# Kernel optimization log

Hardware: AMD Instinct MI355X
Metric: run time of the kernel (lower is better)

Reference implementation:

```python
import jax, jax.numpy as jnp
import numpy as np

B, L, D = 4, 512, 768          # batch, seq, d_model
NL, DI, N, K, R = 12, 1536, 16, 4, 48  # layers, d_inner, d_state, d_conv, dt_rank
V, P = 50257, 1024             # vocab, positions
EPS = 1e-5


def setup_inputs() -> dict:
    key = jax.random.key(0)
    ks = jax.random.split(key, 12)
    p = lambda i, shape, s=0.02: jax.random.normal(ks[i], shape, jnp.float32) * s
    return {
        "input_ids": jax.random.randint(ks[0], (B, L), 0, V),
        "wte": p(1, (V, D)),
        "wpe": p(2, (P, D)),
        "ln_g": jnp.ones((NL, D), jnp.float32),
        "ln_b": jnp.zeros((NL, D), jnp.float32),
        "in_W": p(3, (NL, 2 * DI, D)),
        "conv_W": p(4, (NL, DI, K), 0.2),
        "conv_b": jnp.zeros((NL, DI), jnp.float32),
        "xp_W": p(5, (NL, R + 2 * N, DI)),
        "dt_W": p(6, (NL, DI, R), 0.1),
        "dt_b": p(7, (NL, DI), 0.5),
        # Mamba S4D-real init: A = -exp(A_log), A_log = log(1..N)
        "A_log": jnp.tile(jnp.log(jnp.arange(1, N + 1, dtype=jnp.float32)), (NL, DI, 1)),
        "Dres": jnp.ones((NL, DI), jnp.float32),
        "out_W": p(8, (NL, D, DI)),
        "nf_g": jnp.ones((D,), jnp.float32),
        "nf_b": jnp.zeros((D,), jnp.float32),
        "fin_g": jnp.ones((D,), jnp.float32),
        "fin_b": jnp.zeros((D,), jnp.float32),
    }


def layer_norm(x, g, b):
    mu = jnp.mean(x, -1, keepdims=True)
    var = jnp.mean((x - mu) ** 2, -1, keepdims=True)
    return (x - mu) * jax.lax.rsqrt(var + EPS) * g + b


def causal_conv(x, w, b):
    # x: (B, L, DI); depthwise causal conv, kernel K, left pad K-1, truncate to L
    xt = jnp.transpose(x, (0, 2, 1))  # (B, DI, L)
    y = jax.lax.conv_general_dilated(
        xt, w[:, None, :], (1,), [(K - 1, 0)],
        feature_group_count=DI, dimension_numbers=("NCH", "OIH", "NCH"))
    return jnp.transpose(y + b[None, :, None], (0, 2, 1))


def selective_scan(u, delta, A, Bm, Cm):
    # u, delta: (B, L, DI); A: (DI, N); Bm, Cm: (B, L, N)
    def step(h, inp):
        u_t, d_t, b_t, c_t = inp  # (B,DI), (B,DI), (B,N), (B,N)
        dA = jnp.exp(d_t[:, :, None] * A)            # (B, DI, N)
        h = h * dA + (d_t * u_t)[:, :, None] * b_t[:, None, :]
        y = jnp.einsum("bdn,bn->bd", h, c_t)
        return h, y

    h0 = jnp.zeros((u.shape[0], DI, N), u.dtype)
    xs = (jnp.swapaxes(u, 0, 1), jnp.swapaxes(delta, 0, 1),
          jnp.swapaxes(Bm, 0, 1), jnp.swapaxes(Cm, 0, 1))
    _, ys = jax.lax.scan(step, h0, xs)               # ys: (L, B, DI)
    return jnp.swapaxes(ys, 0, 1)


def mamba_mixer(x, inW, cW, cb, xpW, dtW, dtb, a_log, dres, outW):
    xz = jnp.einsum("bld,ed->ble", x, inW)           # (B, L, 2*DI)
    xi, z = jnp.split(xz, 2, axis=-1)
    xi = jax.nn.silu(causal_conv(xi, cW, cb))
    dbl = jnp.einsum("bld,ed->ble", xi, xpW)         # (B, L, R+2N)
    dt, Bm, Cm = dbl[..., :R], dbl[..., R:R + N], dbl[..., R + N:]
    delta = jax.nn.softplus(jnp.einsum("blr,dr->bld", dt, dtW) + dtb)
    A = -jnp.exp(a_log)
    y = selective_scan(xi, delta, A, Bm, Cm) + xi * dres
    y = y * jax.nn.silu(z)
    return jnp.einsum("ble,de->bld", y, outW)


def reference(input_ids, wte, wpe, ln_g, ln_b, in_W, conv_W, conv_b, xp_W,
              dt_W, dt_b, A_log, Dres, out_W, nf_g, nf_b, fin_g, fin_b):
    emb = wte[input_ids] + wpe[: input_ids.shape[1]]  # (B, L, D); dropout=identity (eval)
    hidden, residual = emb, None
    for i in range(NL):
        residual = hidden if residual is None else hidden + residual
        h = layer_norm(residual, ln_g[i], ln_b[i])
        hidden = mamba_mixer(h, in_W[i], conv_W[i], conv_b[i], xp_W[i],
                             dt_W[i], dt_b[i], A_log[i], Dres[i], out_W[i])
    residual = hidden + residual
    out = layer_norm(residual, nf_g, nf_b)   # MixerModel.norm_f
    return layer_norm(out, fin_g, fin_b)     # decoder self.norm
```

## Files before the change

### kernel.cpp

```cpp
#include <hip/hip_runtime.h>

#define BB 4
#define LL 512
#define DD 768
#define NLAYER 12
#define DI 1536
#define NS 16
#define KC 4
#define RR 48
#define MROWS (BB*LL)
#define E2 (2*DI)
#define EPSV 1e-5f
#define CH2 16
#define LC2 (LL/CH2)

typedef __attribute__((ext_vector_type(8))) short bf16x8;
typedef __attribute__((ext_vector_type(4))) float f32x4;

#define GLL16(g, l) __builtin_amdgcn_global_load_lds( \
    (const __attribute__((address_space(1))) void*)(g), \
    (__attribute__((address_space(3))) void*)(l), 16, 0, 0)

__device__ inline ushort f2bf(float f) {
  union { float f; unsigned u; } v; v.f = f;
  unsigned u = v.u;
  unsigned r = (u + 0x7fffu + ((u >> 16) & 1u)) >> 16;
  return (ushort)r;
}
__device__ inline float bf2f(ushort u) {
  union { unsigned u; float f; } v; v.u = ((unsigned)u) << 16; return v.f;
}

__global__ __launch_bounds__(256) void k_embed(const int* __restrict__ ids,
    const float* __restrict__ wte, const float* __restrict__ wpe,
    float* __restrict__ resid) {
  const int nd4 = DD / 4;
  int i = blockIdx.x * 256 + threadIdx.x;
  if (i >= MROWS * nd4) return;
  int m = i / nd4, d4 = i - m * nd4;
  int l = m & (LL - 1);
  int tok = ids[m];
  float4 a = ((const float4*)wte)[(size_t)tok * nd4 + d4];
  float4 b = ((const float4*)wpe)[(size_t)l * nd4 + d4];
  float4 o; o.x = a.x + b.x; o.y = a.y + b.y; o.z = a.z + b.z; o.w = a.w + b.w;
  ((float4*)resid)[i] = o;
}

__device__ inline float block_sum(float v, volatile float* red) {
  #pragma unroll
  for (int o = 32; o > 0; o >>= 1) v += __shfl_down(v, o);
  if ((threadIdx.x & 63) == 0) red[threadIdx.x >> 6] = v;
  __syncthreads();
  float t = red[0] + red[1] + red[2] + red[3];
  __syncthreads();
  return t;
}

__global__ __launch_bounds__(256) void k_ln(const float* __restrict__ h0,
    const float* __restrict__ h1,
    float* __restrict__ resid, const float* __restrict__ g, const float* __restrict__ b,
    ushort* __restrict__ hbf, int addHidden) {
  __shared__ float red[4];
  int m = blockIdx.x, t = threadIdx.x;
  size_t base = (size_t)m * DD;
  float x0 = resid[base + t], x1 = resid[base + t + 256], x2 = resid[base + t + 512];
  if (addHidden) {
    x0 += h0[base + t]       + h1[base + t];
    x1 += h0[base + t + 256] + h1[base + t + 256];
    x2 += h0[base + t + 512] + h1[base + t + 512];
    resid[base + t] = x0; resid[base + t + 256] = x1; resid[base + t + 512] = x2;
  }
  float S  = block_sum(x0 + x1 + x2, red);
  float S2 = block_sum(x0*x0 + x1*x1 + x2*x2, red);
  float mu = S * (1.f / DD);
  float var = S2 * (1.f / DD) - mu * mu;
  float rs = rsqrtf(var + EPSV);
  hbf[base + t]       = f2bf((x0 - mu) * rs * g[t]       + b[t]);
  hbf[base + t + 256] = f2bf((x1 - mu) * rs * g[t + 256] + b[t + 256]);
  hbf[base + t + 512] = f2bf((x2 - mu) * rs * g[t + 512] + b[t + 512]);
}

template<int OM>
__global__ __launch_bounds__(256) void k_gemm128(const ushort* __restrict__ A,
    const ushort* __restrict__ Bw, void* __restrict__ Cv, int N, int K, int kSteps) {
  __shared__ ushort lA[128 * 32];
  __shared__ ushort lB[128 * 32];
  int tid = threadIdx.x;
  int wid = tid >> 6, lane = tid & 63;
  int tm = blockIdx.y * 128, tn = blockIdx.x * 128;
  int kBase = blockIdx.z * kSteps * 32;
  int wr = (wid >> 1) * 64, wc = (wid & 1) * 64;
  int fr = lane & 15, kg = lane >> 4;
  int srow = lane >> 2;
  int scol = (lane & 3) * 8;
  f32x4 acc[4][4];
  #pragma unroll
  for (int mi = 0; mi < 4; ++mi)
    #pragma unroll
    for (int ni = 0; ni < 4; ++ni)
      acc[mi][ni] = {0.f, 0.f, 0.f, 0.f};

  int rs0 = wid * 2, rs1 = wid * 2 + 1;
  for (int ks = 0; ks < kSteps; ++ks) {
    int k0 = kBase + ks * 32;
    GLL16(A  + (size_t)(tm + rs0 * 16 + srow) * K + k0 + scol, &lA[rs0 * 512]);
    GLL16(A  + (size_t)(tm + rs1 * 16 + srow) * K + k0 + scol, &lA[rs1 * 512]);
    GLL16(Bw + (size_t)(tn + rs0 * 16 + srow) * K + k0 + scol, &lB[rs0 * 512]);
    GLL16(Bw + (size_t)(tn + rs1 * 16 + srow) * K + k0 + scol, &lB[rs1 * 512]);
    __syncthreads();
    bf16x8 af[4], bf[4];
    #pragma unroll
    for (int mi = 0; mi < 4; ++mi)
      af[mi] = *(const bf16x8*)&lA[(wr + mi * 16 + fr) * 32 + kg * 8];
    #pragma unroll
    for (int ni = 0; ni < 4; ++ni)
      bf[ni] = *(const bf16x8*)&lB[(wc + ni * 16 + fr) * 32 + kg * 8];
    #pragma unroll
    for (int mi = 0; mi < 4; ++mi)
      #pragma unroll
      for (int ni = 0; ni < 4; ++ni)
        acc[mi][ni] = __builtin_amdgcn_mfma_f32_16x16x32_bf16(af[mi], bf[ni], acc[mi][ni], 0, 0, 0);
    __syncthreads();
  }
  int crow0 = tm + wr + kg * 4;
  int ccol0 = tn + wc + fr;
  if (OM == 0) {
    float* C = (float*)Cv + (size_t)blockIdx.z * ((size_t)gridDim.y * 128) * N;
    #pragma unroll
    for (int mi = 0; mi < 4; ++mi)
      #pragma unroll
      for (int ni = 0; ni < 4; ++ni)
        #pragma unroll
        for (int j = 0; j < 4; ++j)
          C[(size_t)(crow0 + mi * 16 + j) * N + ccol0 + ni * 16] = acc[mi][ni][j];
  } else {
    ushort* C = (ushort*)Cv;
    #pragma unroll
    for (int mi = 0; mi < 4; ++mi)
      #pragma unroll
      for (int ni = 0; ni < 4; ++ni)
        #pragma unroll
        for (int j = 0; j < 4; ++j)
          C[(size_t)(crow0 + mi * 16 + j) * N + ccol0 + ni * 16] = f2bf(acc[mi][ni][j]);
  }
}

__global__ __launch_bounds__(256) void k_gemm64_part(const ushort* __restrict__ A,
    const ushort* __restrict__ Bw, float* __restrict__ Cp, int N, int K, int kSteps) {
  __shared__ short lA[64][40];
  __shared__ short lB[64][40];
  int tid = threadIdx.x;
  int tm = blockIdx.y * 64, tn = blockIdx.x * 64;
  int kBase = blockIdx.z * kSteps * 32;
  int M = gridDim.y * 64;
  float* C = Cp + (size_t)blockIdx.z * M * N;
  int wid = tid >> 6, lane = tid & 63;
  int wr = (wid >> 1) * 32, wc = (wid & 1) * 32;
  int fr = lane & 15, kg = lane >> 4;
  int ldr = tid >> 2, ldc = (tid & 3) * 8;
  f32x4 acc[2][2];
  #pragma unroll
  for (int mi = 0; mi < 2; ++mi)
    #pragma unroll
    for (int ni = 0; ni < 2; ++ni)
      acc[mi][ni] = {0.f, 0.f, 0.f, 0.f};

  for (int ks = 0; ks < kSteps; ++ks) {
    int k0 = kBase + ks * 32;
    __syncthreads();
    bf16x8 va = *(const bf16x8*)(A + (size_t)(tm + ldr) * K + k0 + ldc);
    short z = 0;
    bf16x8 vb = {z, z, z, z, z, z, z, z};
    int brow = tn + ldr;
    if (brow < N) vb = *(const bf16x8*)(Bw + (size_t)brow * K + k0 + ldc);
    *(bf16x8*)&lA[ldr][ldc] = va;
    *(bf16x8*)&lB[ldr][ldc] = vb;
    __syncthreads();
    bf16x8 a0 = *(const bf16x8*)&lA[wr + fr][kg * 8];
    bf16x8 a1 = *(const bf16x8*)&lA[wr + 16 + fr][kg * 8];
    bf16x8 b0 = *(const bf16x8*)&lB[wc + fr][kg * 8];
    bf16x8 b1 = *(const bf16x8*)&lB[wc + 16 + fr][kg * 8];
    acc[0][0] = __builtin_amdgcn_mfma_f32_16x16x32_bf16(a0, b0, acc[0][0], 0, 0, 0);
    acc[0][1] = __builtin_amdgcn_mfma_f32_16x16x32_bf16(a0, b1, acc[0][1], 0, 0, 0);
    acc[1][0] = __builtin_amdgcn_mfma_f32_16x16x32_bf16(a1, b0, acc[1][0], 0, 0, 0);
    acc[1][1] = __builtin_amdgcn_mfma_f32_16x16x32_bf16(a1, b1, acc[1][1], 0, 0, 0);
  }
  int crow0 = tm + wr + kg * 4;
  int ccol0 = tn + wc + fr;
  #pragma unroll
  for (int mi = 0; mi < 2; ++mi)
    #pragma unroll
    for (int ni = 0; ni < 2; ++ni) {
      int cc = ccol0 + ni * 16;
      if (cc < N) {
        #pragma unroll
        for (int j = 0; j < 4; ++j)
          C[(size_t)(crow0 + mi * 16 + j) * N + cc] = acc[mi][ni][j];
      }
    }
}

__global__ __launch_bounds__(256) void k_gemm64_dt(const ushort* __restrict__ A,
    const ushort* __restrict__ Bw, float* __restrict__ delta,
    const float* __restrict__ dtb, int N, int K) {
  __shared__ short lA[64][40];
  __shared__ short lB[64][40];
  int tid = threadIdx.x;
  int tm = blockIdx.y * 64, tn = blockIdx.x * 64;
  int wid = tid >> 6, lane = tid & 63;
  int wr = (wid >> 1) * 32, wc = (wid & 1) * 32;
  int fr = lane & 15, kg = lane >> 4;
  int ldr = tid >> 2, ldc = (tid & 3) * 8;
  f32x4 acc[2][2];
  #pragma unroll
  for (int mi = 0; mi < 2; ++mi)
    #pragma unroll
    for (int ni = 0; ni < 2; ++ni)
      acc[mi][ni] = {0.f, 0.f, 0.f, 0.f};

  for (int k0 = 0; k0 < K; k0 += 32) {
    __syncthreads();
    bf16x8 va = *(const bf16x8*)(A + (size_t)(tm + ldr) * K + k0 + ldc);
    bf16x8 vb = *(const bf16x8*)(Bw + (size_t)(tn + ldr) * K + k0 + ldc);
    *(bf16x8*)&lA[ldr][ldc] = va;
    *(bf16x8*)&lB[ldr][ldc] = vb;
    __syncthreads();
    bf16x8 a0 = *(const bf16x8*)&lA[wr + fr][kg * 8];
    bf16x8 a1 = *(const bf16x8*)&lA[wr + 16 + fr][kg * 8];
    bf16x8 b0 = *(const bf16x8*)&lB[wc + fr][kg * 8];
    bf16x8 b1 = *(const bf16x8*)&lB[wc + 16 + fr][kg * 8];
    acc[0][0] = __builtin_amdgcn_mfma_f32_16x16x32_bf16(a0, b0, acc[0][0], 0, 0, 0);
    acc[0][1] = __builtin_amdgcn_mfma_f32_16x16x32_bf16(a0, b1, acc[0][1], 0, 0, 0);
    acc[1][0] = __builtin_amdgcn_mfma_f32_16x16x32_bf16(a1, b0, acc[1][0], 0, 0, 0);
    acc[1][1] = __builtin_amdgcn_mfma_f32_16x16x32_bf16(a1, b1, acc[1][1], 0, 0, 0);
  }
  int crow0 = tm + wr + kg * 4;
  int ccol0 = tn + wc + fr;
  #pragma unroll
  for (int mi = 0; mi < 2; ++mi)
    #pragma unroll
    for (int ni = 0; ni < 2; ++ni) {
      int cc = ccol0 + ni * 16;
      #pragma unroll
      for (int j = 0; j < 4; ++j) {
        float x = acc[mi][ni][j] + dtb[cc];
        float sp = (x > 20.f) ? x : log1pf(__expf(x));
        delta[(size_t)(crow0 + mi * 16 + j) * N + cc] = sp;
      }
    }
}

__global__ __launch_bounds__(256) void k_conv(const ushort* __restrict__ xz,
    const float* __restrict__ cW, const float* __restrict__ cb,
    ushort* __restrict__ xibf, int layer) {
  int i = blockIdx.x * 256 + threadIdx.x;
  if (i >= MROWS * DI) return;
  int c = i % DI;
  int m = i / DI;
  int l = m & (LL - 1);
  const float* w = cW + ((size_t)layer * DI + c) * KC;
  float w0 = w[0], w1 = w[1], w2 = w[2], w3 = w[3];
  float acc = cb[(size_t)layer * DI + c];
  if (l >= 3) {
    size_t base = (size_t)(m - 3) * E2 + c;
    acc += bf2f(xz[base]) * w0 + bf2f(xz[base + E2]) * w1 +
           bf2f(xz[base + 2 * E2]) * w2 + bf2f(xz[base + 3 * E2]) * w3;
  } else {
    #pragma unroll
    for (int k = 0; k < KC; ++k) {
      int ll = l - (KC - 1) + k;
      if (ll >= 0) acc += bf2f(xz[(size_t)(m - (KC - 1) + k) * E2 + c]) *
                          ((k == 0) ? w0 : (k == 1) ? w1 : (k == 2) ? w2 : w3);
    }
  }
  float sg = 1.f / (1.f + __expf(-acc));
  xibf[i] = f2bf(acc * sg);
}

__global__ __launch_bounds__(256) void k_cvt4(const float* __restrict__ s,
    ushort* __restrict__ d, int n4) {
  int i = blockIdx.x * 256 + threadIdx.x;
  if (i >= n4) return;
  float4 v = ((const float4*)s)[i];
  ushort4 o = { f2bf(v.x), f2bf(v.y), f2bf(v.z), f2bf(v.w) };
  ((ushort4*)d)[i] = o;
}

__global__ __launch_bounds__(256) void k_cvt_dtw(const float* __restrict__ s,
    ushort* __restrict__ d, int nRows) {
  int i = blockIdx.x * 256 + threadIdx.x;
  if (i >= nRows * 64) return;
  int r = i >> 6, c = i & 63;
  d[i] = (c < RR) ? f2bf(s[(size_t)r * RR + c]) : (ushort)0;
}

__global__ __launch_bounds__(256) void k_comb_xp(const float* __restrict__ part,
    float* __restrict__ dblb, ushort* __restrict__ dtbf) {
  int i = blockIdx.x * 256 + threadIdx.x;
  if (i >= MROWS * 80) return;
  const int S = MROWS * 80;
  float s = part[i] + part[i + S] + part[i + 2 * S] + part[i + 3 * S];
  dblb[i] = s;
  int m = i / 80, c = i - m * 80;
  if (c < RR) dtbf[(size_t)m * 64 + c] = f2bf(s);
  else if (c < 64) dtbf[(size_t)m * 64 + c] = 0;
}

__global__ __launch_bounds__(256) void k_scan_f(const float* __restrict__ delta,
    const ushort* __restrict__ ubf, const float* __restrict__ dblb,
    const ushort* __restrict__ xz, const float* __restrict__ A_log,
    const float* __restrict__ Dres, ushort* __restrict__ ybf, int layer) {
  __shared__ float shH[16 * 257];
  __shared__ float shP[16 * 257];
  int tid = threadIdx.x;
  int dloc = tid & 15, chunk = tid >> 4;
  int d = blockIdx.x * 16 + dloc;
  int b = blockIdx.y;
  float an[16];
  {
    const float4* a4 = (const float4*)(A_log + ((size_t)layer * DI + d) * NS);
    #pragma unroll
    for (int q = 0; q < 4; ++q) {
      float4 v = a4[q];
      an[4*q]   = -__expf(v.x); an[4*q+1] = -__expf(v.y);
      an[4*q+2] = -__expf(v.z); an[4*q+3] = -__expf(v.w);
    }
  }
  int l0 = chunk * LC2;
  size_t rowd0 = ((size_t)b * LL + l0) * DI + d;
  size_t rowb0 = ((size_t)b * LL + l0) * 80 + RR;

  float h[16], pr[16];
  #pragma unroll
  for (int n = 0; n < 16; ++n) { h[n] = 0.f; pr[n] = 1.f; }
  {
    size_t rd = rowd0, rb = rowb0;
    float dl = delta[rd];
    float uv = bf2f(ubf[rd]);
    float4 b0 = *(const float4*)(dblb + rb),     b1 = *(const float4*)(dblb + rb + 4);
    float4 b2 = *(const float4*)(dblb + rb + 8), b3 = *(const float4*)(dblb + rb + 12);
    for (int l = 0; l < LC2; ++l) {
      float dlc = dl, uvc = uv;
      float4 c0 = b0, c1 = b1, c2 = b2, c3 = b3;
      if (l + 1 < LC2) {
        rd += DI; rb += 80;
        dl = delta[rd]; uv = bf2f(ubf[rd]);
        b0 = *(const float4*)(dblb + rb);     b1 = *(const float4*)(dblb + rb + 4);
        b2 = *(const float4*)(dblb + rb + 8); b3 = *(const float4*)(dblb + rb + 12);
      }
      float du = dlc * uvc;
      float Bv[16] = { c0.x, c0.y, c0.z, c0.w, c1.x, c1.y, c1.z, c1.w,
                       c2.x, c2.y, c2.z, c2.w, c3.x, c3.y, c3.z, c3.w };
      #pragma unroll
      for (int n = 0; n < 16; ++n) {
        float a = __expf(dlc * an[n]);
        h[n] = h[n] * a + du * Bv[n];
        pr[n] *= a;
      }
    }
  }
  {
    int base = dloc * 257 + chunk * 16;
    #pragma unroll
    for (int n = 0; n < 16; ++n) { shH[base + n] = h[n]; shP[base + n] = pr[n]; }
  }
  __syncthreads();

  {
    int n2 = tid & 15, dl2 = tid >> 4;
    float hh = 0.f;
    int base = dl2 * 257;
    for (int c = 0; c < CH2; ++c) {
      int idx = base + c * 16 + n2;
      float t = shH[idx], p = shP[idx];
      shH[idx] = hh;
      hh = t + p * hh;
    }
  }
  __syncthreads();

  {
    int base = dloc * 257 + chunk * 16;
    #pragma unroll
    for (int n = 0; n < 16; ++n) h[n] = shH[base + n];
  }
  float dresv = Dres[(size_t)layer * DI + d];
  {
    size_t rd = rowd0, rb = rowb0;
    size_t rz = ((size_t)b * LL + l0) * E2 + DI + d;
    float dl = delta[rd];
    float uv = bf2f(ubf[rd]);
    float4 b0 = *(const float4*)(dblb + rb),      b1 = *(const float4*)(dblb + rb + 4);
    float4 b2 = *(const float4*)(dblb + rb + 8),  b3 = *(const float4*)(dblb + rb + 12);
    float4 e0 = *(const float4*)(dblb + rb + 16), e1 = *(const float4*)(dblb + rb + 20);
    float4 e2 = *(const float4*)(dblb + rb + 24), e3 = *(const float4*)(dblb + rb + 28);
    for (int l = 0; l < LC2; ++l) {
      float dlc = dl, uvc = uv;
      float4 c0 = b0, c1 = b1, c2 = b2, c3 = b3;
      float4 f0 = e0, f1 = e1, f2 = e2, f3 = e3;
      size_t rdc = rd, rzc = rz;
      if (l + 1 < LC2) {
        rd += DI; rb += 80; rz += E2;
        dl = delta[rd]; uv = bf2f(ubf[rd]);
        b0 = *(const float4*)(dblb + rb);      b1 = *(const float4*)(dblb + rb + 4);
        b2 = *(const float4*)(dblb + rb + 8);  b3 = *(const float4*)(dblb + rb + 12);
        e0 = *(const float4*)(dblb + rb + 16); e1 = *(const float4*)(dblb + rb + 20);
        e2 = *(const float4*)(dblb + rb + 24); e3 = *(const float4*)(dblb + rb + 28);
      }
      float du = dlc * uvc;
      float Bv[16] = { c0.x, c0.y, c0.z, c0.w, c1.x, c1.y, c1.z, c1.w,
                       c2.x, c2.y, c2.z, c2.w, c3.x, c3.y, c3.z, c3.w };
      float Cv[16] = { f0.x, f0.y, f0.z, f0.w, f1.x, f1.y, f1.z, f1.w,
                       f2.x, f2.y, f2.z, f2.w, f3.x, f3.y, f3.z, f3.w };
      float y = 0.f;
      #pragma unroll
      for (int n = 0; n < 16; ++n) {
        float a = __expf(dlc * an[n]);
        h[n] = h[n] * a + du * Bv[n];
        y += h[n] * Cv[n];
      }
      float zv = bf2f(xz[rzc]);
      float yt = y + uvc * dresv;
      float sg = 1.f / (1.f + __expf(-zv));
      ybf[rdc] = f2bf(yt * (zv * sg));
    }
  }
}

__global__ __launch_bounds__(256) void k_final(const float* __restrict__ resid,
    const float* __restrict__ h0, const float* __restrict__ h1,
    const float* __restrict__ nfg, const float* __restrict__ nfb,
    const float* __restrict__ fig, const float* __restrict__ fib,
    float* __restrict__ out) {
  __shared__ float red[4];
  int m = blockIdx.x, t = threadIdx.x;
  size_t base = (size_t)m * DD;
  float x0 = resid[base + t]       + h0[base + t]       + h1[base + t];
  float x1 = resid[base + t + 256] + h0[base + t + 256] + h1[base + t + 256];
  float x2 = resid[base + t + 512] + h0[base + t + 512] + h1[base + t + 512];
  float S  = block_sum(x0 + x1 + x2, red);
  float S2 = block_sum(x0*x0 + x1*x1 + x2*x2, red);
  float mu = S * (1.f / DD);
  float var = S2 * (1.f / DD) - mu * mu;
  float rs = rsqrtf(var + EPSV);
  float t0 = (x0 - mu) * rs * nfg[t]       + nfb[t];
  float t1 = (x1 - mu) * rs * nfg[t + 256] + nfb[t + 256];
  float t2 = (x2 - mu) * rs * nfg[t + 512] + nfb[t + 512];
  S  = block_sum(t0 + t1 + t2, red);
  S2 = block_sum(t0*t0 + t1*t1 + t2*t2, red);
  mu = S * (1.f / DD);
  var = S2 * (1.f / DD) - mu * mu;
  rs = rsqrtf(var + EPSV);
  out[base + t]       = (t0 - mu) * rs * fig[t]       + fib[t];
  out[base + t + 256] = (t1 - mu) * rs * fig[t + 256] + fib[t + 256];
  out[base + t + 512] = (t2 - mu) * rs * fig[t + 512] + fib[t + 512];
}

extern "C" void kernel_launch(void* const* d_in, const int* in_sizes, int n_in,
                              void* d_out, int out_size, void* d_ws, size_t ws_size,
                              hipStream_t stream) {
  const int*   ids    = (const int*)  d_in[0];
  const float* wte    = (const float*)d_in[1];
  const float* wpe    = (const float*)d_in[2];
  const float* ln_g   = (const float*)d_in[3];
  const float* ln_b   = (const float*)d_in[4];
  const float* in_W   = (const float*)d_in[5];
  const float* conv_W = (const float*)d_in[6];
  const float* conv_b = (const float*)d_in[7];
  const float* xp_W   = (const float*)d_in[8];
  const float* dt_W   = (const float*)d_in[9];
  const float* dt_b   = (const float*)d_in[10];
  const float* A_log  = (const float*)d_in[11];
  const float* Dres   = (const float*)d_in[12];
  const float* out_W  = (const float*)d_in[13];
  const float* nf_g   = (const float*)d_in[14];
  const float* nf_b   = (const float*)d_in[15];
  const float* fin_g  = (const float*)d_in[16];
  const float* fin_b  = (const float*)d_in[17];

  char* p = (char*)d_ws;
  auto take = [&](size_t bytes) {
    char* r = p; p += (bytes + 255) & ~(size_t)255; return r;
  };
  float*  resid  = (float*) take((size_t)MROWS * DD * 4);
  float*  hidP   = (float*) take((size_t)2 * MROWS * DD * 4);
  ushort* h_bf   = (ushort*)take((size_t)MROWS * DD * 2);
  ushort* xz     = (ushort*)take((size_t)MROWS * E2 * 2);
  ushort* xibf   = (ushort*)take((size_t)MROWS * DI * 2);
  float*  xpPart = (float*) take((size_t)4 * MROWS * 80 * 4);
  float*  dblb   = (float*) take((size_t)MROWS * 80 * 4);
  ushort* dtbf   = (ushort*)take((size_t)MROWS * 64 * 2);
  float*  delta  = (float*) take((size_t)MROWS * DI * 4);
  ushort* ybf    = (ushort*)take((size_t)MROWS * DI * 2);
  ushort* wInBf  = (ushort*)take((size_t)NLAYER * E2 * DD * 2);
  ushort* wXpBf  = (ushort*)take((size_t)NLAYER * 80 * DI * 2);
  ushort* wDtBf  = (ushort*)take((size_t)NLAYER * DI * 64 * 2);
  ushort* wOutBf = (ushort*)take((size_t)NLAYER * DD * DI * 2);

  k_cvt4<<<(NLAYER * E2 * DD / 4 + 255) / 256, 256, 0, stream>>>(in_W, wInBf, NLAYER * E2 * DD / 4);
  k_cvt4<<<(NLAYER * 80 * DI / 4 + 255) / 256, 256, 0, stream>>>(xp_W, wXpBf, NLAYER * 80 * DI / 4);
  k_cvt_dtw<<<(NLAYER * DI * 64 + 255) / 256, 256, 0, stream>>>(dt_W, wDtBf, NLAYER * DI);
  k_cvt4<<<(NLAYER * DD * DI / 4 + 255) / 256, 256, 0, stream>>>(out_W, wOutBf, NLAYER * DD * DI / 4);

  k_embed<<<(MROWS * (DD / 4) + 255) / 256, 256, 0, stream>>>(ids, wte, wpe, resid);

  for (int i = 0; i < NLAYER; ++i) {
    k_ln<<<MROWS, 256, 0, stream>>>(hidP, hidP + (size_t)MROWS * DD, resid,
                                    ln_g + (size_t)i * DD, ln_b + (size_t)i * DD,
                                    h_bf, i > 0 ? 1 : 0);

    { dim3 g(E2 / 128, MROWS / 128, 1);
      k_gemm128<1><<<g, 256, 0, stream>>>(h_bf, wInBf + (size_t)i * E2 * DD,
                                          (void*)xz, E2, DD, DD / 32); }

    k_conv<<<((MROWS * DI) + 255) / 256, 256, 0, stream>>>(xz, conv_W, conv_b, xibf, i);

    { dim3 g(2, MROWS / 64, 4);
      k_gemm64_part<<<g, 256, 0, stream>>>(xibf, wXpBf + (size_t)i * 80 * DI,
                                           xpPart, 80, DI, DI / 32 / 4); }

    k_comb_xp<<<(MROWS * 80 + 255) / 256, 256, 0, stream>>>(xpPart, dblb, dtbf);

    { dim3 g(DI / 64, MROWS / 64);
      k_gemm64_dt<<<g, 256, 0, stream>>>(dtbf, wDtBf + (size_t)i * DI * 64,
                                         delta, dt_b + (size_t)i * DI, DI, 64); }

    { dim3 g(DI / 16, BB);
      k_scan_f<<<g, 256, 0, stream>>>(delta, xibf, dblb, xz, A_log, Dres, ybf, i); }

    { dim3 g(DD / 128, MROWS / 128, 2);
      k_gemm128<0><<<g, 256, 0, stream>>>(ybf, wOutBf + (size_t)i * DD * DI,
                                          (void*)hidP, DD, DI, DI / 32 / 2); }
  }

  k_final<<<MROWS, 256, 0, stream>>>(resid, hidP, hidP + (size_t)MROWS * DD,
                                     nf_g, nf_b, fin_g, fin_b, (float*)d_out);
}
```

Baseline: 1.563 ms.

## Widen GEMM K-tile to 64 with XOR-swizzled LDS and unify small GEMMs

The 128x128 GEMM now stages a 64-wide K slice per iteration, using XOR-swizzled LDS addressing to avoid bank conflicts, and runs two MFMA sub-steps per barrier pair. The x_proj and dt_proj GEMMs reuse this kernel: x_proj gets a split-K of 8 with clamped B rows, and dt_proj fuses the bias and softplus into a new epilogue mode. The aim is fewer barriers per FLOP and dropping the slower 64x64 kernels. The scan's exp becomes a hardware exp2 with log2(e) folded into A. The x_proj tile pads N=80 up to 128, which wastes MFMA work, and the dt_proj GEMM launches fewer blocks.

```diff
diff --git a/kernel.cpp b/kernel.cpp
--- a/kernel.cpp
+++ b/kernel.cpp
@@ -13,6 +13,7 @@
 #define EPSV 1e-5f
 #define CH2 16
 #define LC2 (LL/CH2)
+#define LOG2E 1.4426950408889634f
 
 typedef __attribute__((ext_vector_type(8))) short bf16x8;
 typedef __attribute__((ext_vector_type(4))) float f32x4;
@@ -20,6 +21,8 @@
 #define GLL16(g, l) __builtin_amdgcn_global_load_lds( \
     (const __attribute__((address_space(1))) void*)(g), \
     (__attribute__((address_space(3))) void*)(l), 16, 0, 0)
+
+__device__ inline float hw_exp2(float x) { return __builtin_amdgcn_exp2f(x); }
 
 __device__ inline ushort f2bf(float f) {
   union { float f; unsigned u; } v; v.f = f;
@@ -82,17 +85,18 @@
 
 template<int OM>
 __global__ __launch_bounds__(256) void k_gemm128(const ushort* __restrict__ A,
-    const ushort* __restrict__ Bw, void* __restrict__ Cv, int N, int K, int kSteps) {
-  __shared__ ushort lA[128 * 32];
-  __shared__ ushort lB[128 * 32];
+    const ushort* __restrict__ Bw, void* __restrict__ Cv, const float* __restrict__ dtb,
+    int N, int K, int kSteps) {
+  __shared__ ushort lA[128 * 64];
+  __shared__ ushort lB[128 * 64];
   int tid = threadIdx.x;
   int wid = tid >> 6, lane = tid & 63;
   int tm = blockIdx.y * 128, tn = blockIdx.x * 128;
-  int kBase = blockIdx.z * kSteps * 32;
+  int kBase = blockIdx.z * kSteps * 64;
   int wr = (wid >> 1) * 64, wc = (wid & 1) * 64;
   int fr = lane & 15, kg = lane >> 4;
-  int srow = lane >> 2;
-  int scol = (lane & 3) * 8;
+  int sR = lane >> 3;
+  int sC = ((lane & 7) ^ sR) * 8;
   f32x4 acc[4][4];
   #pragma unroll
   for (int mi = 0; mi < 4; ++mi)
@@ -100,26 +104,36 @@
     for (int ni = 0; ni < 4; ++ni)
       acc[mi][ni] = {0.f, 0.f, 0.f, 0.f};
 
-  int rs0 = wid * 2, rs1 = wid * 2 + 1;
   for (int ks = 0; ks < kSteps; ++ks) {
-    int k0 = kBase + ks * 32;
-    GLL16(A  + (size_t)(tm + rs0 * 16 + srow) * K + k0 + scol, &lA[rs0 * 512]);
-    GLL16(A  + (size_t)(tm + rs1 * 16 + srow) * K + k0 + scol, &lA[rs1 * 512]);
-    GLL16(Bw + (size_t)(tn + rs0 * 16 + srow) * K + k0 + scol, &lB[rs0 * 512]);
-    GLL16(Bw + (size_t)(tn + rs1 * 16 + srow) * K + k0 + scol, &lB[rs1 * 512]);
+    int k0 = kBase + ks * 64;
+    #pragma unroll
+    for (int i = 0; i < 4; ++i) {
+      int r0 = wid * 32 + i * 8;
+      GLL16(A + (size_t)(tm + r0 + sR) * K + k0 + sC, &lA[r0 * 64]);
+      int brow = tn + r0 + sR;
+      if (brow > N - 1) brow = N - 1;
+      GLL16(Bw + (size_t)brow * K + k0 + sC, &lB[r0 * 64]);
+    }
     __syncthreads();
-    bf16x8 af[4], bf[4];
-    #pragma unroll
-    for (int mi = 0; mi < 4; ++mi)
-      af[mi] = *(const bf16x8*)&lA[(wr + mi * 16 + fr) * 32 + kg * 8];
-    #pragma unroll
-    for (int ni = 0; ni < 4; ++ni)
-      bf[ni] = *(const bf16x8*)&lB[(wc + ni * 16 + fr) * 32 + kg * 8];
-    #pragma unroll
-    for (int mi = 0; mi < 4; ++mi)
-      #pragma unroll
-      for (int ni = 0; ni < 4; ++ni)
-        acc[mi][ni] = __builtin_amdgcn_mfma_f32_16x16x32_bf16(af[mi], bf[ni], acc[mi][ni], 0, 0, 0);
+    #pragma unroll
+    for (int ks2 = 0; ks2 < 2; ++ks2) {
+      bf16x8 af[4], bfr[4];
+      #pragma unroll
+      for (int mi = 0; mi < 4; ++mi) {
+        int row = wr + mi * 16 + fr;
+        af[mi] = *(const bf16x8*)&lA[row * 64 + (((ks2 * 4 + kg) ^ (fr & 7)) * 8)];
+      }
+      #pragma unroll
+      for (int ni = 0; ni < 4; ++ni) {
+        int row = wc + ni * 16 + fr;
+        bfr[ni] = *(const bf16x8*)&lB[row * 64 + (((ks2 * 4 + kg) ^ (fr & 7)) * 8)];
+      }
+      #pragma unroll
+      for (int mi = 0; mi < 4; ++mi)
+        #pragma unroll
+        for (int ni = 0; ni < 4; ++ni)
+          acc[mi][ni] = __builtin_amdgcn_mfma_f32_16x16x32_bf16(af[mi], bfr[ni], acc[mi][ni], 0, 0, 0);
+    }
     __syncthreads();
   }
   int crow0 = tm + wr + kg * 4;
@@ -129,125 +143,45 @@
     #pragma unroll
     for (int mi = 0; mi < 4; ++mi)
       #pragma unroll
-      for (int ni = 0; ni < 4; ++ni)
-        #pragma unroll
-        for (int j = 0; j < 4; ++j)
-          C[(size_t)(crow0 + mi * 16 + j) * N + ccol0 + ni * 16] = acc[mi][ni][j];
+      for (int ni = 0; ni < 4; ++ni) {
+        int cc = ccol0 + ni * 16;
+        if (cc < N) {
+          #pragma unroll
+          for (int j = 0; j < 4; ++j)
+            C[(size_t)(crow0 + mi * 16 + j) * N + cc] = acc[mi][ni][j];
+        }
+      }
+  } else if (OM == 1) {
+    ushort* C = (ushort*)Cv;
+    #pragma unroll
+    for (int mi = 0; mi < 4; ++mi)
+      #pragma unroll
+      for (int ni = 0; ni < 4; ++ni) {
+        int cc = ccol0 + ni * 16;
+        if (cc < N) {
+          #pragma unroll
+          for (int j = 0; j < 4; ++j)
+            C[(size_t)(crow0 + mi * 16 + j) * N + cc] = f2bf(acc[mi][ni][j]);
+        }
+      }
   } else {
-    ushort* C = (ushort*)Cv;
+    float* C = (float*)Cv;
     #pragma unroll
     for (int mi = 0; mi < 4; ++mi)
       #pragma unroll
-      for (int ni = 0; ni < 4; ++ni)
-        #pragma unroll
-        for (int j = 0; j < 4; ++j)
-          C[(size_t)(crow0 + mi * 16 + j) * N + ccol0 + ni * 16] = f2bf(acc[mi][ni][j]);
-  }
-}
-
-__global__ __launch_bounds__(256) void k_gemm64_part(const ushort* __restrict__ A,
-    const ushort* __restrict__ Bw, float* __restrict__ Cp, int N, int K, int kSteps) {
-  __shared__ short lA[64][40];
-  __shared__ short lB[64][40];
-  int tid = threadIdx.x;
-  int tm = blockIdx.y * 64, tn = blockIdx.x * 64;
-  int kBase = blockIdx.z * kSteps * 32;
-  int M = gridDim.y * 64;
-  float* C = Cp + (size_t)blockIdx.z * M * N;
-  int wid = tid >> 6, lane = tid & 63;
-  int wr = (wid >> 1) * 32, wc = (wid & 1) * 32;
-  int fr = lane & 15, kg = lane >> 4;
-  int ldr = tid >> 2, ldc = (tid & 3) * 8;
-  f32x4 acc[2][2];
-  #pragma unroll
-  for (int mi = 0; mi < 2; ++mi)
-    #pragma unroll
-    for (int ni = 0; ni < 2; ++ni)
-      acc[mi][ni] = {0.f, 0.f, 0.f, 0.f};
-
-  for (int ks = 0; ks < kSteps; ++ks) {
-    int k0 = kBase + ks * 32;
-    __syncthreads();
-    bf16x8 va = *(const bf16x8*)(A + (size_t)(tm + ldr) * K + k0 + ldc);
-    short z = 0;
-    bf16x8 vb = {z, z, z, z, z, z, z, z};
-    int brow = tn + ldr;
-    if (brow < N) vb = *(const bf16x8*)(Bw + (size_t)brow * K + k0 + ldc);
-    *(bf16x8*)&lA[ldr][ldc] = va;
-    *(bf16x8*)&lB[ldr][ldc] = vb;
-    __syncthreads();
-    bf16x8 a0 = *(const bf16x8*)&lA[wr + fr][kg * 8];
-    bf16x8 a1 = *(const bf16x8*)&lA[wr + 16 + fr][kg * 8];
-    bf16x8 b0 = *(const bf16x8*)&lB[wc + fr][kg * 8];
-    bf16x8 b1 = *(const bf16x8*)&lB[wc + 16 + fr][kg * 8];
-    acc[0][0] = __builtin_amdgcn_mfma_f32_16x16x32_bf16(a0, b0, acc[0][0], 0, 0, 0);
-    acc[0][1] = __builtin_amdgcn_mfma_f32_16x16x32_bf16(a0, b1, acc[0][1], 0, 0, 0);
-    acc[1][0] = __builtin_amdgcn_mfma_f32_16x16x32_bf16(a1, b0, acc[1][0], 0, 0, 0);
-    acc[1][1] = __builtin_amdgcn_mfma_f32_16x16x32_bf16(a1, b1, acc[1][1], 0, 0, 0);
-  }
-  int crow0 = tm + wr + kg * 4;
-  int ccol0 = tn + wc + fr;
-  #pragma unroll
-  for (int mi = 0; mi < 2; ++mi)
-    #pragma unroll
-    for (int ni = 0; ni < 2; ++ni) {
-      int cc = ccol0 + ni * 16;
-      if (cc < N) {
-        #pragma unroll
-        for (int j = 0; j < 4; ++j)
-          C[(size_t)(crow0 + mi * 16 + j) * N + cc] = acc[mi][ni][j];
-      }
-    }
-}
-
-__global__ __launch_bounds__(256) void k_gemm64_dt(const ushort* __restrict__ A,
-    const ushort* __restrict__ Bw, float* __restrict__ delta,
-    const float* __restrict__ dtb, int N, int K) {
-  __shared__ short lA[64][40];
-  __shared__ short lB[64][40];
-  int tid = threadIdx.x;
-  int tm = blockIdx.y * 64, tn = blockIdx.x * 64;
-  int wid = tid >> 6, lane = tid & 63;
-  int wr = (wid >> 1) * 32, wc = (wid & 1) * 32;
-  int fr = lane & 15, kg = lane >> 4;
-  int ldr = tid >> 2, ldc = (tid & 3) * 8;
-  f32x4 acc[2][2];
-  #pragma unroll
-  for (int mi = 0; mi < 2; ++mi)
-    #pragma unroll
-    for (int ni = 0; ni < 2; ++ni)
-      acc[mi][ni] = {0.f, 0.f, 0.f, 0.f};
-
-  for (int k0 = 0; k0 < K; k0 += 32) {
-    __syncthreads();
-    bf16x8 va = *(const bf16x8*)(A + (size_t)(tm + ldr) * K + k0 + ldc);
-    bf16x8 vb = *(const bf16x8*)(Bw + (size_t)(tn + ldr) * K + k0 + ldc);
-    *(bf16x8*)&lA[ldr][ldc] = va;
-    *(bf16x8*)&lB[ldr][ldc] = vb;
-    __syncthreads();
-    bf16x8 a0 = *(const bf16x8*)&lA[wr + fr][kg * 8];
-    bf16x8 a1 = *(const bf16x8*)&lA[wr + 16 + fr][kg * 8];
-    bf16x8 b0 = *(const bf16x8*)&lB[wc + fr][kg * 8];
-    bf16x8 b1 = *(const bf16x8*)&lB[wc + 16 + fr][kg * 8];
-    acc[0][0] = __builtin_amdgcn_mfma_f32_16x16x32_bf16(a0, b0, acc[0][0], 0, 0, 0);
-    acc[0][1] = __builtin_amdgcn_mfma_f32_16x16x32_bf16(a0, b1, acc[0][1], 0, 0, 0);
-    acc[1][0] = __builtin_amdgcn_mfma_f32_16x16x32_bf16(a1, b0, acc[1][0], 0, 0, 0);
-    acc[1][1] = __builtin_amdgcn_mfma_f32_16x16x32_bf16(a1, b1, acc[1][1], 0, 0, 0);
-  }
-  int crow0 = tm + wr + kg * 4;
-  int ccol0 = tn + wc + fr;
-  #pragma unroll
-  for (int mi = 0; mi < 2; ++mi)
-    #pragma unroll
-    for (int ni = 0; ni < 2; ++ni) {
-      int cc = ccol0 + ni * 16;
-      #pragma unroll
-      for (int j = 0; j < 4; ++j) {
-        float x = acc[mi][ni][j] + dtb[cc];
-        float sp = (x > 20.f) ? x : log1pf(__expf(x));
-        delta[(size_t)(crow0 + mi * 16 + j) * N + cc] = sp;
-      }
-    }
+      for (int ni = 0; ni < 4; ++ni) {
+        int cc = ccol0 + ni * 16;
+        if (cc < N) {
+          float bv = dtb[cc];
+          #pragma unroll
+          for (int j = 0; j < 4; ++j) {
+            float x = acc[mi][ni][j] + bv;
+            float sp = (x > 20.f) ? x : log1pf(__expf(x));
+            C[(size_t)(crow0 + mi * 16 + j) * N + cc] = sp;
+          }
+        }
+      }
+  }
 }
 
 __global__ __launch_bounds__(256) void k_conv(const ushort* __restrict__ xz,
@@ -299,7 +233,9 @@
   int i = blockIdx.x * 256 + threadIdx.x;
   if (i >= MROWS * 80) return;
   const int S = MROWS * 80;
-  float s = part[i] + part[i + S] + part[i + 2 * S] + part[i + 3 * S];
+  float s = 0.f;
+  #pragma unroll
+  for (int z = 0; z < 8; ++z) s += part[i + z * S];
   dblb[i] = s;
   int m = i / 80, c = i - m * 80;
   if (c < RR) dtbf[(size_t)m * 64 + c] = f2bf(s);
@@ -322,8 +258,8 @@
     #pragma unroll
     for (int q = 0; q < 4; ++q) {
       float4 v = a4[q];
-      an[4*q]   = -__expf(v.x); an[4*q+1] = -__expf(v.y);
-      an[4*q+2] = -__expf(v.z); an[4*q+3] = -__expf(v.w);
+      an[4*q]   = -__expf(v.x) * LOG2E; an[4*q+1] = -__expf(v.y) * LOG2E;
+      an[4*q+2] = -__expf(v.z) * LOG2E; an[4*q+3] = -__expf(v.w) * LOG2E;
     }
   }
   int l0 = chunk * LC2;
@@ -353,7 +289,7 @@
                        c2.x, c2.y, c2.z, c2.w, c3.x, c3.y, c3.z, c3.w };
       #pragma unroll
       for (int n = 0; n < 16; ++n) {
-        float a = __expf(dlc * an[n]);
+        float a = hw_exp2(dlc * an[n]);
         h[n] = h[n] * a + du * Bv[n];
         pr[n] *= a;
       }
@@ -415,7 +351,7 @@
       float y = 0.f;
       #pragma unroll
       for (int n = 0; n < 16; ++n) {
-        float a = __expf(dlc * an[n]);
+        float a = hw_exp2(dlc * an[n]);
         h[n] = h[n] * a + du * Bv[n];
         y += h[n] * Cv[n];
       }
@@ -487,7 +423,7 @@
   ushort* h_bf   = (ushort*)take((size_t)MROWS * DD * 2);
   ushort* xz     = (ushort*)take((size_t)MROWS * E2 * 2);
   ushort* xibf   = (ushort*)take((size_t)MROWS * DI * 2);
-  float*  xpPart = (float*) take((size_t)4 * MROWS * 80 * 4);
+  float*  xpPart = (float*) take((size_t)8 * MROWS * 80 * 4);
   float*  dblb   = (float*) take((size_t)MROWS * 80 * 4);
   ushort* dtbf   = (ushort*)take((size_t)MROWS * 64 * 2);
   float*  delta  = (float*) take((size_t)MROWS * DI * 4);
@@ -511,26 +447,26 @@
 
     { dim3 g(E2 / 128, MROWS / 128, 1);
       k_gemm128<1><<<g, 256, 0, stream>>>(h_bf, wInBf + (size_t)i * E2 * DD,
-                                          (void*)xz, E2, DD, DD / 32); }
+                                          (void*)xz, nullptr, E2, DD, DD / 64); }
 
     k_conv<<<((MROWS * DI) + 255) / 256, 256, 0, stream>>>(xz, conv_W, conv_b, xibf, i);
 
-    { dim3 g(2, MROWS / 64, 4);
-      k_gemm64_part<<<g, 256, 0, stream>>>(xibf, wXpBf + (size_t)i * 80 * DI,
-                                           xpPart, 80, DI, DI / 32 / 4); }
+    { dim3 g(1, MROWS / 128, 8);
+      k_gemm128<0><<<g, 256, 0, stream>>>(xibf, wXpBf + (size_t)i * 80 * DI,
+                                          (void*)xpPart, nullptr, 80, DI, DI / 64 / 8); }
 
     k_comb_xp<<<(MROWS * 80 + 255) / 256, 256, 0, stream>>>(xpPart, dblb, dtbf);
 
-    { dim3 g(DI / 64, MROWS / 64);
-      k_gemm64_dt<<<g, 256, 0, stream>>>(dtbf, wDtBf + (size_t)i * DI * 64,
-                                         delta, dt_b + (size_t)i * DI, DI, 64); }
+    { dim3 g(DI / 128, MROWS / 128, 1);
+      k_gemm128<2><<<g, 256, 0, stream>>>(dtbf, wDtBf + (size_t)i * DI * 64,
+                                          (void*)delta, dt_b + (size_t)i * DI, DI, 64, 1); }
 
     { dim3 g(DI / 16, BB);
       k_scan_f<<<g, 256, 0, stream>>>(delta, xibf, dblb, xz, A_log, Dres, ybf, i); }
 
     { dim3 g(DD / 128, MROWS / 128, 2);
       k_gemm128<0><<<g, 256, 0, stream>>>(ybf, wOutBf + (size_t)i * DD * DI,
-                                          (void*)hidP, DD, DI, DI / 32 / 2); }
+                                          (void*)hidP, nullptr, DD, DI, DI / 64 / 2); }
   }
 
   k_final<<<MROWS, 256, 0, stream>>>(resid, hidP, hidP + (size_t)MROWS * DD,
```

After: 1.596 ms. 1.02x slower.
